# Optimization experiments

Measured on AMD Instinct MI355X. Metric: run time of the kernel, lower is better.

## Reference

```python
import jax, jax.numpy as jnp
import numpy as np
from jax import lax

WINDOW_SIZES = (3, 5, 7)
FEATURE_SCALES = (1.0, 1.0, 0.5, 0.001)  # mean, variance, skewness, kurtosis
EPS = 1e-8


def _gaussian_window(k: int) -> jnp.ndarray:
    sigma = k / 6.0
    coords = jnp.arange(k, dtype=jnp.float32) - (k // 2)
    g = jnp.exp(-coords ** 2 / (2.0 * sigma ** 2))
    g = g / g.sum()
    g2 = g[None, :] * g[:, None]
    return g2 / g2.sum()  # [k, k]


def _dwconv(x: jnp.ndarray, w2d: jnp.ndarray) -> jnp.ndarray:
    # depthwise conv, same gaussian kernel for every channel, SAME-style padding k//2
    c = x.shape[1]
    k = w2d.shape[-1]
    kernel = jnp.broadcast_to(w2d[None, None], (c, 1, k, k)).astype(x.dtype)
    p = k // 2
    return lax.conv_general_dilated(
        x, kernel, window_strides=(1, 1), padding=[(p, p), (p, p)],
        dimension_numbers=('NCHW', 'OIHW', 'NCHW'), feature_group_count=c)


def _stat_features(x: jnp.ndarray, w2d: jnp.ndarray):
    mean = _dwconv(x, w2d)
    var = jnp.clip(_dwconv(x * x, w2d) - mean * mean, EPS, None)
    xc = x - mean
    m3 = _dwconv(xc * xc * xc, w2d)
    m4 = _dwconv(xc * xc * xc * xc, w2d)
    std = jnp.sqrt(var)
    skew = m3 / (std * std * std + EPS)
    kurt = m4 / (var * var + EPS)
    return (mean, var, skew, kurt)


def setup_inputs() -> dict:
    key = jax.random.key(0)
    k1, k2 = jax.random.split(key)
    pred = jax.random.normal(k1, (16, 3, 512, 512), dtype=jnp.float32)
    target = jax.random.normal(k2, (16, 3, 512, 512), dtype=jnp.float32)
    return {"pred": pred, "target": target}


def reference(pred, target):
    loss_weight = 1.0
    total = jnp.asarray(0.0, dtype=pred.dtype)
    num_features = 0
    for k in WINDOW_SIZES:
        w2d = _gaussian_window(k)
        pf = _stat_features(pred, w2d)
        tf = _stat_features(target, w2d)
        for p_feat, t_feat, scale in zip(pf, tf, FEATURE_SCALES):
            total = total + jnp.abs(p_feat - t_feat).mean() * scale
            num_features += 1
    return loss_weight * total / num_features
```

## Files before the change

### kernel.cpp

```cpp
#include <hip/hip_runtime.h>
#include <math.h>


static constexpr int H = 512, W = 512, PLANES = 48;
static constexpr float EPSF = 1e-8f;

__global__ void init_acc_kernel(double* acc) {
    if (threadIdx.x < 4) acc[threadIdx.x] = 0.0;
}

__global__ void final_kernel(const double* __restrict__ acc, float* __restrict__ out) {
    if (threadIdx.x == 0) {
        const double npix = (double)PLANES * H * W;
        double tot = acc[0] + acc[1] + 0.5 * acc[2] + 0.001 * acc[3];
        out[0] = (float)(tot / (npix * 12.0));
    }
}

__device__ __forceinline__ float bperm(int addr, float v) {
    return __int_as_float(__builtin_amdgcn_ds_bpermute(addr, __float_as_int(v)));
}

template <int K, int BAND, int D, int DX, int NSTRIP>
__global__ __launch_bounds__(256)
void stat_kernel(const float* __restrict__ pred, const float* __restrict__ targ,
                 double* __restrict__ acc) {
    constexpr int R  = K / 2;
    constexpr int OW = 64 - 4 * R;
    constexpr int NBAND = H / BAND;
    constexpr int T  = BAND + 4 * R;
    constexpr int Tp = ((T + D - 1) / D) * D;

    const int wv    = threadIdx.x >> 6;
    const int wid   = blockIdx.x * 4 + wv;
    const int band  = wid % NBAND;
    const int tmp   = wid / NBAND;
    const int strip = tmp % NSTRIP;
    const int plane = tmp / NSTRIP;
    const int t     = threadIdx.x & 63;
    const int gc0   = strip * OW - 2 * R + t;
    const int y0    = band * BAND - 2 * R;

    const bool  iva     = (unsigned)gc0 < (unsigned)W;
    const float colmask = iva ? 1.f : 0.f;
    const float emask   = (t >= 2 * R && t < 2 * R + OW && gc0 < W) ? 1.f : 0.f;

    int adr[K];
#pragma unroll
    for (int j = 0; j < K; ++j) adr[j] = (t - R + j) << 2;

    float g[K];
    {
        const float sigma = (float)K / 6.0f;
        const float inv2s2 = 1.0f / (2.0f * sigma * sigma);
        float s = 0.0f;
#pragma unroll
        for (int i = 0; i < K; ++i) {
            float c = (float)(i - K / 2);
            g[i] = expf(-c * c * inv2s2);
            s += g[i];
        }
#pragma unroll
        for (int i = 0; i < K; ++i)
            g[i] = __int_as_float(__builtin_amdgcn_readfirstlane(__float_as_int(g[i] / s)));
    }

    const float* src0 = pred + (size_t)plane * H * W + gc0;
    const float* src1 = targ + (size_t)plane * H * W + gc0;

    auto loadrow = [&](int s, int y) -> float {
        float v = 0.f;
        if (iva && (unsigned)y < (unsigned)H)
            v = (s == 0 ? src0 : src1)[(long)y << 9];
        return v;
    };

    float mn[2][D], msq[2][D], m3a[2][D], m4a[2][D], xr[2][DX];
    float featp[4];
    float sums[4] = {0.f, 0.f, 0.f, 0.f};
    float pf[2] = { loadrow(0, y0), loadrow(1, y0) };

    for (int yy = 0; yy < Tp; yy += D) {
#pragma unroll
        for (int u = 0; u < D; ++u) {
            const int i = yy + u;
            const int y = y0 + i;
            const float rmask = (((unsigned)(y - R) < (unsigned)H) ? 1.f : 0.f) * colmask;
#pragma unroll
            for (int s = 0; s < 2; ++s) {
                const float x = pf[s];
                pf[s] = loadrow(s, y + 1);
                xr[s][u % DX] = x;

                float w[K];
#pragma unroll
                for (int j = 0; j < K; ++j) w[j] = (j == R) ? x : bperm(adr[j], x);
                float hx = 0.f, hq = 0.f;
#pragma unroll
                for (int j = 0; j < K; ++j) { hx += g[j] * w[j]; hq += g[j] * (w[j] * w[j]); }

#pragma unroll
                for (int d = 0; d < K; ++d) {
                    const int sl = (u + d - R + 2 * D) % D;
                    if (d == K - 1) { mn[s][sl] = g[d] * hx; msq[s][sl] = g[d] * hq; }
                    else           { mn[s][sl] += g[d] * hx; msq[s][sl] += g[d] * hq; }
                }

                const float xold  = xr[s][(u - R + 2 * DX) % DX];
                const float mean1 = mn[s][(u - R + 2 * D) % D];
                const float xcm   = (xold - mean1) * rmask;

                float wc[K];
#pragma unroll
                for (int j = 0; j < K; ++j) wc[j] = (j == R) ? xcm : bperm(adr[j], xcm);
                float v3 = 0.f, v4 = 0.f;
#pragma unroll
                for (int j = 0; j < K; ++j) {
                    const float c2 = wc[j] * wc[j];
                    v3 += g[j] * (c2 * wc[j]);
                    v4 += g[j] * (c2 * c2);
                }

#pragma unroll
                for (int d = 0; d < K; ++d) {
                    const int sl = (u + d - 2 * R + 2 * D) % D;
                    if (d == K - 1) { m3a[s][sl] = g[d] * v3; m4a[s][sl] = g[d] * v4; }
                    else           { m3a[s][sl] += g[d] * v3; m4a[s][sl] += g[d] * v4; }
                }

                if (i >= 4 * R && i < T) {
                    const int se = (u - 2 * R + 2 * D) % D;
                    const float mean = mn[s][se];
                    const float var  = fmaxf(msq[s][se] - mean * mean, EPSF);
                    const float sd   = sqrtf(var);
                    const float skew = __fdividef(m3a[s][se], sd * var + EPSF);
                    const float kurt = __fdividef(m4a[s][se], var * var + EPSF);
                    if (s == 0) {
                        featp[0] = mean; featp[1] = var; featp[2] = skew; featp[3] = kurt;
                    } else {
                        sums[0] += fabsf(featp[0] - mean);
                        sums[1] += fabsf(featp[1] - var);
                        sums[2] += fabsf(featp[2] - skew);
                        sums[3] += fabsf(featp[3] - kurt);
                    }
                }
            }
        }
    }

    __shared__ float red[4][4];
#pragma unroll
    for (int f = 0; f < 4; ++f) {
        float v = sums[f] * emask;
#pragma unroll
        for (int off = 32; off > 0; off >>= 1) v += __shfl_down(v, off, 64);
        if (t == 0) red[wv][f] = v;
    }
    __syncthreads();
    if (threadIdx.x < 4) {
        float v = red[0][threadIdx.x] + red[1][threadIdx.x]
                + red[2][threadIdx.x] + red[3][threadIdx.x];
        atomicAdd(&acc[threadIdx.x], (double)v);
    }
}

extern "C" void kernel_launch(void* const* d_in, const int* in_sizes, int n_in,
                              void* d_out, int out_size, void* d_ws, size_t ws_size,
                              hipStream_t stream) {
    const float* pred = (const float*)d_in[0];
    const float* targ = (const float*)d_in[1];
    double* acc = (double*)d_ws;
    float* out = (float*)d_out;

    init_acc_kernel<<<1, 64, 0, stream>>>(acc);

    stat_kernel<3, 32,  4, 2,  9><<<dim3(PLANES *  9 * 16 / 4), 256, 0, stream>>>(pred, targ, acc);
    stat_kernel<5, 32,  7, 7, 10><<<dim3(PLANES * 10 * 16 / 4), 256, 0, stream>>>(pred, targ, acc);
    stat_kernel<7, 64, 10, 5, 10><<<dim3(PLANES * 10 *  8 / 4), 256, 0, stream>>>(pred, targ, acc);

    final_kernel<<<1, 64, 0, stream>>>(acc, out);
}
```

Baseline: 451.9 us.

## Software-pipeline cross-lane permutes one row ahead and double band heights

The ds_bpermute horizontal-neighbour gathers for both the raw row and the centred row are now issued one iteration before their values are consumed. Their LDS-path latency can then overlap with the current row's arithmetic, and the global load prefetch moves two rows ahead. The ring buffers grow by one slot and the central-moment pipeline is delayed by a row to match. Band heights are doubled so the vertical halo recompute is amortised over more rows, at the cost of fewer waves and more registers per thread.

```diff
diff --git a/kernel.cpp b/kernel.cpp
--- a/kernel.cpp
+++ b/kernel.cpp
@@ -21,15 +21,16 @@
     return __int_as_float(__builtin_amdgcn_ds_bpermute(addr, __float_as_int(v)));
 }
 
-template <int K, int BAND, int D, int DX, int NSTRIP>
+template <int K, int BAND, int D, int NSTRIP>
 __global__ __launch_bounds__(256)
 void stat_kernel(const float* __restrict__ pred, const float* __restrict__ targ,
                  double* __restrict__ acc) {
     constexpr int R  = K / 2;
     constexpr int OW = 64 - 4 * R;
     constexpr int NBAND = H / BAND;
-    constexpr int T  = BAND + 4 * R;
+    constexpr int T  = BAND + 4 * R + 1;
     constexpr int Tp = ((T + D - 1) / D) * D;
+    static_assert(D >= 3 * R + 2, "ring depth");
 
     const int wv    = threadIdx.x >> 6;
     const int wid   = blockIdx.x * 4 + wv;
@@ -75,10 +76,20 @@
         return v;
     };
 
-    float mn[2][D], msq[2][D], m3a[2][D], m4a[2][D], xr[2][DX];
+    float mn[2][D] = {}, msq[2][D] = {}, m3a[2][D] = {}, m4a[2][D] = {}, xr[2][D] = {};
+    float w[2][K];
+    float wc[2][K] = {};
+    float pf[2];
     float featp[4];
     float sums[4] = {0.f, 0.f, 0.f, 0.f};
-    float pf[2] = { loadrow(0, y0), loadrow(1, y0) };
+
+#pragma unroll
+    for (int s = 0; s < 2; ++s) {
+        const float x0 = loadrow(s, y0);
+#pragma unroll
+        for (int j = 0; j < K; ++j) w[s][j] = (j == R) ? x0 : bperm(adr[j], x0);
+        pf[s] = loadrow(s, y0 + 1);
+    }
 
     for (int yy = 0; yy < Tp; yy += D) {
 #pragma unroll
@@ -86,50 +97,54 @@
             const int i = yy + u;
             const int y = y0 + i;
             const float rmask = (((unsigned)(y - R) < (unsigned)H) ? 1.f : 0.f) * colmask;
+            const bool emit = (i >= 4 * R + 1) && (i < T);
 #pragma unroll
             for (int s = 0; s < 2; ++s) {
-                const float x = pf[s];
-                pf[s] = loadrow(s, y + 1);
-                xr[s][u % DX] = x;
-
-                float w[K];
-#pragma unroll
-                for (int j = 0; j < K; ++j) w[j] = (j == R) ? x : bperm(adr[j], x);
+                const float x = w[s][R];
                 float hx = 0.f, hq = 0.f;
 #pragma unroll
-                for (int j = 0; j < K; ++j) { hx += g[j] * w[j]; hq += g[j] * (w[j] * w[j]); }
+                for (int j = 0; j < K; ++j) {
+                    hx += g[j] * w[s][j];
+                    hq += g[j] * (w[s][j] * w[s][j]);
+                }
+                const float xnext = pf[s];
+                pf[s] = loadrow(s, y + 2);
+#pragma unroll
+                for (int j = 0; j < K; ++j)
+                    w[s][j] = (j == R) ? xnext : bperm(adr[j], xnext);
 
 #pragma unroll
                 for (int d = 0; d < K; ++d) {
-                    const int sl = (u + d - R + 2 * D) % D;
+                    const int sl = (u + d - R + 3 * D) % D;
                     if (d == K - 1) { mn[s][sl] = g[d] * hx; msq[s][sl] = g[d] * hq; }
                     else           { mn[s][sl] += g[d] * hx; msq[s][sl] += g[d] * hq; }
                 }
+                xr[s][u] = x;
 
-                const float xold  = xr[s][(u - R + 2 * DX) % DX];
-                const float mean1 = mn[s][(u - R + 2 * D) % D];
+                const float xold  = xr[s][(u - R + 3 * D) % D];
+                const float mean1 = mn[s][(u - R + 3 * D) % D];
                 const float xcm   = (xold - mean1) * rmask;
 
-                float wc[K];
-#pragma unroll
-                for (int j = 0; j < K; ++j) wc[j] = (j == R) ? xcm : bperm(adr[j], xcm);
                 float v3 = 0.f, v4 = 0.f;
 #pragma unroll
                 for (int j = 0; j < K; ++j) {
-                    const float c2 = wc[j] * wc[j];
-                    v3 += g[j] * (c2 * wc[j]);
+                    const float c2 = wc[s][j] * wc[s][j];
+                    v3 += g[j] * (c2 * wc[s][j]);
                     v4 += g[j] * (c2 * c2);
                 }
+#pragma unroll
+                for (int j = 0; j < K; ++j)
+                    wc[s][j] = (j == R) ? xcm : bperm(adr[j], xcm);
 
 #pragma unroll
                 for (int d = 0; d < K; ++d) {
-                    const int sl = (u + d - 2 * R + 2 * D) % D;
+                    const int sl = (u + d - 2 * R - 1 + 3 * D) % D;
                     if (d == K - 1) { m3a[s][sl] = g[d] * v3; m4a[s][sl] = g[d] * v4; }
                     else           { m3a[s][sl] += g[d] * v3; m4a[s][sl] += g[d] * v4; }
                 }
 
-                if (i >= 4 * R && i < T) {
-                    const int se = (u - 2 * R + 2 * D) % D;
+                if (emit) {
+                    const int se = (u - 2 * R - 1 + 3 * D) % D;
                     const float mean = mn[s][se];
                     const float var  = fmaxf(msq[s][se] - mean * mean, EPSF);
                     const float sd   = sqrtf(var);
@@ -174,9 +189,9 @@
 
     init_acc_kernel<<<1, 64, 0, stream>>>(acc);
 
-    stat_kernel<3, 32,  4, 2,  9><<<dim3(PLANES *  9 * 16 / 4), 256, 0, stream>>>(pred, targ, acc);
-    stat_kernel<5, 32,  7, 7, 10><<<dim3(PLANES * 10 * 16 / 4), 256, 0, stream>>>(pred, targ, acc);
-    stat_kernel<7, 64, 10, 5, 10><<<dim3(PLANES * 10 *  8 / 4), 256, 0, stream>>>(pred, targ, acc);
+    stat_kernel<3,  64,  5,  9><<<dim3(48 *  9 * 8 / 4), 256, 0, stream>>>(pred, targ, acc);
+    stat_kernel<5,  64,  8, 10><<<dim3(48 * 10 * 8 / 4), 256, 0, stream>>>(pred, targ, acc);
+    stat_kernel<7, 128, 11, 10><<<dim3(48 * 10 * 4 / 4), 256, 0, stream>>>(pred, targ, acc);
 
     final_kernel<<<1, 64, 0, stream>>>(acc, out);
 }
```

After: 454.2 us. About the same (+0.5%).

## Fuse three window-size stat kernels into one pass sharing row loads

Applied to the files above, without the earlier changes.

Replaces three separately launched per-window-size kernels with a single kernel that handles windows 3, 5 and 7 in the same row sweep, using one common strip width (52) and taller bands (128 rows). Each loaded pixel feeds all three window pipelines, so global reads and launch overhead are paid once instead of three times. In exchange, register pressure rises a lot because all three sets of rolling accumulators (up to 12 deep) stay live, which risks spills and lower occupancy, and the narrower strips for K=3 add halo redundancy.

```diff
diff --git a/kernel.cpp b/kernel.cpp
--- a/kernel.cpp
+++ b/kernel.cpp
@@ -4,6 +4,10 @@
 
 static constexpr int H = 512, W = 512, PLANES = 48;
 static constexpr float EPSF = 1e-8f;
+static constexpr int BAND = 128, NBAND = H / BAND;
+static constexpr int OW = 52, NSTRIP = 10;
+static constexpr int T  = BAND + 12;
+static constexpr int Tp = ((T + 11) / 12) * 12;
 
 __global__ void init_acc_kernel(double* acc) {
     if (threadIdx.x < 4) acc[threadIdx.x] = 0.0;
@@ -21,16 +25,68 @@
     return __int_as_float(__builtin_amdgcn_ds_bpermute(addr, __float_as_int(v)));
 }
 
-template <int K, int BAND, int D, int DX, int NSTRIP>
+template <int K, int DK>
+__device__ __forceinline__ void kstep(
+    int u, int t, float x, float rmask, bool okEmit,
+    const float* __restrict__ g, const float (&xrs)[4],
+    float (&mn)[DK], float (&msq)[DK], float (&m3a)[DK], float (&m4a)[DK],
+    float (&featp)[4], float (&sums)[4], int s)
+{
+    constexpr int R = K / 2;
+    float w[K];
+#pragma unroll
+    for (int j = 0; j < K; ++j)
+        w[j] = (j == R) ? x : bperm((t - R + j) << 2, x);
+    float hx = 0.f, hq = 0.f;
+#pragma unroll
+    for (int j = 0; j < K; ++j) { hx += g[j] * w[j]; hq += g[j] * (w[j] * w[j]); }
+#pragma unroll
+    for (int d = 0; d < K; ++d) {
+        const int sl = (u + d - R + 4 * DK) % DK;
+        if (d == K - 1) { mn[sl] = g[d] * hx; msq[sl] = g[d] * hq; }
+        else            { mn[sl] += g[d] * hx; msq[sl] += g[d] * hq; }
+    }
+    const float xold  = xrs[(u - R + 8) & 3];
+    const float mean1 = mn[(u - R + 4 * DK) % DK];
+    const float xcm   = (xold - mean1) * rmask;
+    float wc[K];
+#pragma unroll
+    for (int j = 0; j < K; ++j)
+        wc[j] = (j == R) ? xcm : bperm((t - R + j) << 2, xcm);
+    float v3 = 0.f, v4 = 0.f;
+#pragma unroll
+    for (int j = 0; j < K; ++j) {
+        const float c2 = wc[j] * wc[j];
+        v3 += g[j] * (c2 * wc[j]);
+        v4 += g[j] * (c2 * c2);
+    }
+#pragma unroll
+    for (int d = 0; d < K; ++d) {
+        const int sl = (u + d - 2 * R + 4 * DK) % DK;
+        if (d == K - 1) { m3a[sl] = g[d] * v3; m4a[sl] = g[d] * v4; }
+        else            { m3a[sl] += g[d] * v3; m4a[sl] += g[d] * v4; }
+    }
+    if (okEmit) {
+        const int se = (u - 2 * R + 4 * DK) % DK;
+        const float mean = mn[se];
+        const float var  = fmaxf(msq[se] - mean * mean, EPSF);
+        const float sd   = sqrtf(var);
+        const float skew = __fdividef(m3a[se], sd * var + EPSF);
+        const float kurt = __fdividef(m4a[se], var * var + EPSF);
+        if (s == 0) {
+            featp[0] = mean; featp[1] = var; featp[2] = skew; featp[3] = kurt;
+        } else {
+            sums[0] += fabsf(featp[0] - mean);
+            sums[1] += fabsf(featp[1] - var);
+            sums[2] += fabsf(featp[2] - skew);
+            sums[3] += fabsf(featp[3] - kurt);
+        }
+    }
+}
+
 __global__ __launch_bounds__(256)
 void stat_kernel(const float* __restrict__ pred, const float* __restrict__ targ,
                  double* __restrict__ acc) {
-    constexpr int R  = K / 2;
-    constexpr int OW = 64 - 4 * R;
-    constexpr int NBAND = H / BAND;
-    constexpr int T  = BAND + 4 * R;
-    constexpr int Tp = ((T + D - 1) / D) * D;
-
     const int wv    = threadIdx.x >> 6;
     const int wid   = blockIdx.x * 4 + wv;
     const int band  = wid % NBAND;
@@ -38,31 +94,28 @@
     const int strip = tmp % NSTRIP;
     const int plane = tmp / NSTRIP;
     const int t     = threadIdx.x & 63;
-    const int gc0   = strip * OW - 2 * R + t;
-    const int y0    = band * BAND - 2 * R;
+    const int gc0   = strip * OW - 6 + t;
+    const int y0    = band * BAND - 6;
 
     const bool  iva     = (unsigned)gc0 < (unsigned)W;
     const float colmask = iva ? 1.f : 0.f;
-    const float emask   = (t >= 2 * R && t < 2 * R + OW && gc0 < W) ? 1.f : 0.f;
+    const float emask   = (t >= 6 && t < 6 + OW && gc0 < W) ? 1.f : 0.f;
 
-    int adr[K];
-#pragma unroll
-    for (int j = 0; j < K; ++j) adr[j] = (t - R + j) << 2;
-
-    float g[K];
+    float g3[3], g5[5], g7[7];
     {
-        const float sigma = (float)K / 6.0f;
-        const float inv2s2 = 1.0f / (2.0f * sigma * sigma);
-        float s = 0.0f;
-#pragma unroll
-        for (int i = 0; i < K; ++i) {
-            float c = (float)(i - K / 2);
-            g[i] = expf(-c * c * inv2s2);
-            s += g[i];
-        }
-#pragma unroll
-        for (int i = 0; i < K; ++i)
-            g[i] = __int_as_float(__builtin_amdgcn_readfirstlane(__float_as_int(g[i] / s)));
+        auto build = [&](float* g, int K) {
+            const float sigma = (float)K / 6.0f;
+            const float inv2s2 = 1.0f / (2.0f * sigma * sigma);
+            float s = 0.0f;
+            for (int i = 0; i < K; ++i) {
+                float c = (float)(i - K / 2);
+                g[i] = expf(-c * c * inv2s2);
+                s += g[i];
+            }
+            for (int i = 0; i < K; ++i)
+                g[i] = __int_as_float(__builtin_amdgcn_readfirstlane(__float_as_int(g[i] / s)));
+        };
+        build(g3, 3); build(g5, 5); build(g7, 7);
     }
 
     const float* src0 = pred + (size_t)plane * H * W + gc0;
@@ -75,75 +128,38 @@
         return v;
     };
 
-    float mn[2][D], msq[2][D], m3a[2][D], m4a[2][D], xr[2][DX];
-    float featp[4];
+    float xr[2][4];
+    float mn3[2][4]  = {}, msq3[2][4]  = {}, m33[2][4]  = {}, m43[2][4]  = {};
+    float mn5[2][12] = {}, msq5[2][12] = {}, m35[2][12] = {}, m45[2][12] = {};
+    float mn7[2][12] = {}, msq7[2][12] = {}, m37[2][12] = {}, m47[2][12] = {};
+    float fp3[4], fp5[4], fp7[4];
     float sums[4] = {0.f, 0.f, 0.f, 0.f};
     float pf[2] = { loadrow(0, y0), loadrow(1, y0) };
+    xr[0][3] = 0.f; xr[1][3] = 0.f; xr[0][2] = 0.f; xr[1][2] = 0.f;
+    xr[0][1] = 0.f; xr[1][1] = 0.f; xr[0][0] = 0.f; xr[1][0] = 0.f;
 
-    for (int yy = 0; yy < Tp; yy += D) {
+    for (int yy = 0; yy < Tp; yy += 12) {
 #pragma unroll
-        for (int u = 0; u < D; ++u) {
+        for (int u = 0; u < 12; ++u) {
             const int i = yy + u;
             const int y = y0 + i;
-            const float rmask = (((unsigned)(y - R) < (unsigned)H) ? 1.f : 0.f) * colmask;
+            const float rm1 = (((unsigned)(y - 1) < (unsigned)H) ? 1.f : 0.f) * colmask;
+            const float rm2 = (((unsigned)(y - 2) < (unsigned)H) ? 1.f : 0.f) * colmask;
+            const float rm3 = (((unsigned)(y - 3) < (unsigned)H) ? 1.f : 0.f) * colmask;
+            const bool e3 = (i >= 8)  && (i < 8 + BAND);
+            const bool e5 = (i >= 10) && (i < 10 + BAND);
+            const bool e7 = (i >= 12) && (i < 12 + BAND);
 #pragma unroll
             for (int s = 0; s < 2; ++s) {
                 const float x = pf[s];
                 pf[s] = loadrow(s, y + 1);
-                xr[s][u % DX] = x;
-
-                float w[K];
-#pragma unroll
-                for (int j = 0; j < K; ++j) w[j] = (j == R) ? x : bperm(adr[j], x);
-                float hx = 0.f, hq = 0.f;
-#pragma unroll
-                for (int j = 0; j < K; ++j) { hx += g[j] * w[j]; hq += g[j] * (w[j] * w[j]); }
-
-#pragma unroll
-                for (int d = 0; d < K; ++d) {
-                    const int sl = (u + d - R + 2 * D) % D;
-                    if (d == K - 1) { mn[s][sl] = g[d] * hx; msq[s][sl] = g[d] * hq; }
-                    else           { mn[s][sl] += g[d] * hx; msq[s][sl] += g[d] * hq; }
-                }
-
-                const float xold  = xr[s][(u - R + 2 * DX) % DX];
-                const float mean1 = mn[s][(u - R + 2 * D) % D];
-                const float xcm   = (xold - mean1) * rmask;
-
-                float wc[K];
-#pragma unroll
-                for (int j = 0; j < K; ++j) wc[j] = (j == R) ? xcm : bperm(adr[j], xcm);
-                float v3 = 0.f, v4 = 0.f;
-#pragma unroll
-                for (int j = 0; j < K; ++j) {
-                    const float c2 = wc[j] * wc[j];
-                    v3 += g[j] * (c2 * wc[j]);
-                    v4 += g[j] * (c2 * c2);
-                }
-
-#pragma unroll
-                for (int d = 0; d < K; ++d) {
-                    const int sl = (u + d - 2 * R + 2 * D) % D;
-                    if (d == K - 1) { m3a[s][sl] = g[d] * v3; m4a[s][sl] = g[d] * v4; }
-                    else           { m3a[s][sl] += g[d] * v3; m4a[s][sl] += g[d] * v4; }
-                }
-
-                if (i >= 4 * R && i < T) {
-                    const int se = (u - 2 * R + 2 * D) % D;
-                    const float mean = mn[s][se];
-                    const float var  = fmaxf(msq[s][se] - mean * mean, EPSF);
-                    const float sd   = sqrtf(var);
-                    const float skew = __fdividef(m3a[s][se], sd * var + EPSF);
-                    const float kurt = __fdividef(m4a[s][se], var * var + EPSF);
-                    if (s == 0) {
-                        featp[0] = mean; featp[1] = var; featp[2] = skew; featp[3] = kurt;
-                    } else {
-                        sums[0] += fabsf(featp[0] - mean);
-                        sums[1] += fabsf(featp[1] - var);
-                        sums[2] += fabsf(featp[2] - skew);
-                        sums[3] += fabsf(featp[3] - kurt);
-                    }
-                }
+                xr[s][u & 3] = x;
+                kstep<3, 4>(u, t, x, rm1, e3, g3, xr[s],
+                            mn3[s], msq3[s], m33[s], m43[s], fp3, sums, s);
+                kstep<5, 12>(u, t, x, rm2, e5, g5, xr[s],
+                             mn5[s], msq5[s], m35[s], m45[s], fp5, sums, s);
+                kstep<7, 12>(u, t, x, rm3, e7, g7, xr[s],
+                             mn7[s], msq7[s], m37[s], m47[s], fp7, sums, s);
             }
         }
     }
@@ -174,9 +190,7 @@
 
     init_acc_kernel<<<1, 64, 0, stream>>>(acc);
 
-    stat_kernel<3, 32,  4, 2,  9><<<dim3(PLANES *  9 * 16 / 4), 256, 0, stream>>>(pred, targ, acc);
-    stat_kernel<5, 32,  7, 7, 10><<<dim3(PLANES * 10 * 16 / 4), 256, 0, stream>>>(pred, targ, acc);
-    stat_kernel<7, 64, 10, 5, 10><<<dim3(PLANES * 10 *  8 / 4), 256, 0, stream>>>(pred, targ, acc);
+    stat_kernel<<<dim3(PLANES * NSTRIP * NBAND / 4), 256, 0, stream>>>(pred, targ, acc);
 
     final_kernel<<<1, 64, 0, stream>>>(acc, out);
 }
```

Result: slower. 649.8 us (+43.8%).
